# Optimization experiments

Hardware: AMD Instinct MI355X
Metric: run time of the kernel (lower is better)

Reference implementation:

```python
import jax, jax.numpy as jnp
import numpy as np

B, N = 2, 2048
TOP_K = 48
NUM_RBF = 16
MAX_REL = 32            # max_relative_feature
NUM_POS = 16            # num_positional_embeddings
EDGE_FEATURES = 128
EDGE_IN = NUM_POS + NUM_RBF * 25  # 416
POS_IN = 2 * MAX_REL + 2          # 66 one-hot classes


def setup_inputs() -> dict:
    key = jax.random.key(0)
    k0, k1, k2, k3 = jax.random.split(key, 4)
    X = jax.random.normal(k0, (B, N, 4, 3), dtype=jnp.float32) * 3.0
    mask = jnp.ones((B, N), dtype=jnp.float32)
    R_idx = jnp.arange(B * N, dtype=jnp.int32).reshape(B, N)
    chain_labels = jax.random.randint(k1, (B, N), 0, 4).astype(jnp.int32)
    W_pos = 0.05 * jax.random.normal(k2, (POS_IN, NUM_POS), dtype=jnp.float32)
    b_pos = jnp.zeros((NUM_POS,), dtype=jnp.float32)
    W_edge = 0.05 * jax.random.normal(k3, (EDGE_IN, EDGE_FEATURES), dtype=jnp.float32)
    b_edge = jnp.zeros((EDGE_FEATURES,), dtype=jnp.float32)
    return {"X": X, "mask": mask, "R_idx": R_idx, "chain_labels": chain_labels,
            "W_pos": W_pos, "b_pos": b_pos, "W_edge": W_edge, "b_edge": b_edge}


def _rbf(D):
    # D: [..., K] -> [..., K, NUM_RBF]
    mu = jnp.linspace(2.0, 22.0, NUM_RBF)        # D_min=2, D_max=22
    sigma = (22.0 - 2.0) / NUM_RBF               # 1.25
    return jnp.exp(-(((D[..., None] - mu) / sigma) ** 2))


def _pair_dist(A, Bc):
    # A, Bc: [B, N, 3] -> [B, N, N]
    return jnp.sqrt(jnp.sum((A[:, :, None, :] - Bc[:, None, :, :]) ** 2, axis=-1) + 1e-6)


def reference(X, mask, R_idx, chain_labels, W_pos, b_pos, W_edge, b_edge):
    # virtual Cbeta from backbone geometry
    b = X[:, :, 1, :] - X[:, :, 0, :]
    c = X[:, :, 2, :] - X[:, :, 1, :]
    a = jnp.cross(b, c, axis=-1)
    Cb = -0.58273431 * a + 0.56802827 * b - 0.54067466 * c + X[:, :, 1, :]
    Ca, Nat, Cat, Oat = X[:, :, 1, :], X[:, :, 0, :], X[:, :, 2, :], X[:, :, 3, :]

    # masked Ca-Ca distances + k nearest neighbors
    mask2 = mask[:, None, :] * mask[:, :, None]
    D = mask2 * _pair_dist(Ca, Ca)
    D_adjust = D + (1.0 - mask2) * jnp.max(D, axis=-1, keepdims=True)
    neg_D, E_idx = jax.lax.top_k(-D_adjust, min(TOP_K, N))  # smallest distances
    D_neighbors = -neg_D                                     # [B, N, K]

    rbfs = [_rbf(D_neighbors)]
    pairs = [(Nat, Nat), (Cat, Cat), (Oat, Oat), (Cb, Cb),
             (Ca, Nat), (Ca, Cat), (Ca, Oat), (Ca, Cb),
             (Nat, Cat), (Nat, Oat), (Nat, Cb), (Cb, Cat), (Cb, Oat), (Oat, Cat),
             (Nat, Ca), (Cat, Ca), (Oat, Ca), (Cb, Ca),
             (Cat, Nat), (Oat, Nat), (Cb, Nat), (Cat, Cb), (Oat, Cb), (Cat, Oat)]
    for A_, B_ in pairs:  # fixed structural set of 24 atom-pair types
        Dab = _pair_dist(A_, B_)                          # [B, N, N]
        Dn = jnp.take_along_axis(Dab, E_idx, axis=2)      # [B, N, K]
        rbfs.append(_rbf(Dn))
    RBF_all = jnp.concatenate(rbfs, axis=-1)              # [B, N, K, 25*NUM_RBF]

    # relative positional / chain features at the gathered neighbors
    offset = R_idx[:, :, None] - R_idx[:, None, :]
    offset = jnp.take_along_axis(offset, E_idx, axis=2)   # [B, N, K]
    d_chains = (chain_labels[:, :, None] == chain_labels[:, None, :]).astype(jnp.int32)
    E_chains = jnp.take_along_axis(d_chains, E_idx, axis=2)

    d = jnp.clip(offset + MAX_REL, 0, 2 * MAX_REL)
    d = d * E_chains + (1 - E_chains) * (2 * MAX_REL + 1)
    d_onehot = jax.nn.one_hot(d, POS_IN, dtype=jnp.float32)  # [B, N, K, 66]
    E_positional = d_onehot @ W_pos + b_pos                  # [B, N, K, 16]

    E = jnp.concatenate((E_positional, RBF_all), axis=-1)    # [B, N, K, 416]
    E = E @ W_edge + b_edge                                  # [B, N, K, 128]
    return E, E_idx
```

## Files before the change

### kernel.cpp

```cpp
#include <hip/hip_runtime.h>
#include <hip/hip_bf16.h>
#include <stdint.h>

#define BB   2
#define NN   2048
#define BN   (BB*NN)
#define KTOP 48
#define EIN  416
#define EF   128

typedef __attribute__((ext_vector_type(8))) short s8v;
typedef __attribute__((ext_vector_type(4))) float f32x4;
typedef __attribute__((ext_vector_type(4))) unsigned int u32x4;
typedef unsigned short u16;
typedef unsigned int u32;
typedef unsigned long long u64;

__device__ __constant__ int cPA[25] = {1,0,2,3,4,1,1,1,1,0,0,0,4,4,3,0,2,3,4,2,3,4,2,3,2};
__device__ __constant__ int cPB[25] = {1,0,2,3,4,0,2,3,4,2,3,4,2,3,2,1,1,1,1,0,0,0,4,4,3};

__device__ __forceinline__ u16 bf16u(float x) {
  __hip_bfloat16 h = __float2bfloat16(x);
  return *reinterpret_cast<u16*>(&h);
}
__device__ __forceinline__ u32 cvtpk(float lo, float hi) {
  u32 r;
  asm("v_cvt_pk_bf16_f32 %0, %1, %2" : "=v"(r) : "v"(lo), "v"(hi));
  return r;
}

__global__ __launch_bounds__(256) void prep_kernel(const float* __restrict__ X,
                                                   const float* __restrict__ W_edge,
                                                   float* __restrict__ atoms5p,
                                                   float* __restrict__ capack4,
                                                   u16* __restrict__ wtf) {
  int tid = blockIdx.x * 256 + threadIdx.x;
  if (tid < EIN * EF) {
    int k = tid >> 7, n = tid & 127;
    wtf[((size_t)(k >> 3)) * 1024 + n * 8 + (k & 7)] = bf16u(W_edge[tid]);
  } else if (tid < EIN * EF + BN) {
    int idx = tid - EIN * EF;
    const float* x = X + (size_t)idx * 12;
    float Nx = x[0], Ny = x[1], Nz = x[2];
    float Cax = x[3], Cay = x[4], Caz = x[5];
    float Cx = x[6], Cy = x[7], Cz = x[8];
    float Ox = x[9], Oy = x[10], Oz = x[11];
    float bx = Cax - Nx, by = Cay - Ny, bz = Caz - Nz;
    float cx = Cx - Cax, cy = Cy - Cay, cz = Cz - Caz;
    float ax = by * cz - bz * cy;
    float ay = bz * cx - bx * cz;
    float az = bx * cy - by * cx;
    float Cbx = -0.58273431f * ax + 0.56802827f * bx - 0.54067466f * cx + Cax;
    float Cby = -0.58273431f * ay + 0.56802827f * by - 0.54067466f * cy + Cay;
    float Cbz = -0.58273431f * az + 0.56802827f * bz - 0.54067466f * cz + Caz;
    f32x4* o = (f32x4*)(atoms5p + (size_t)idx * 20);
    o[0] = (f32x4){Nx, Ny, Nz, 0.f};
    o[1] = (f32x4){Cax, Cay, Caz, 0.f};
    o[2] = (f32x4){Cx, Cy, Cz, 0.f};
    o[3] = (f32x4){Ox, Oy, Oz, 0.f};
    o[4] = (f32x4){Cbx, Cby, Cbz, 0.f};
    *(f32x4*)(capack4 + (size_t)idx * 4) = (f32x4){Cax, Cay, Caz, 0.f};
  }
}

__device__ __forceinline__ u32 blockExclScan(u32 v, u32* scanw, int t) {
  int lane = t & 63, w = t >> 6;
  u32 inc = v;
#pragma unroll
  for (int off = 1; off < 64; off <<= 1) {
    u32 o = __shfl_up(inc, off);
    if (lane >= off) inc += o;
  }
  if (lane == 63) scanw[w] = inc;
  __syncthreads();
  u32 base = 0;
  for (int ww = 0; ww < w; ++ww) base += scanw[ww];
  __syncthreads();
  return base + inc - v;
}

template<int NB, bool CHKPREF>
__device__ __forceinline__ void radix_round(u32* hist, u32* scanw, u32* selinfo, int t,
                                            const u32* kv, u32 pref, int prefShift,
                                            int binShift, u32 binMask, u32 r) {
  const int PB = NB / 256;
#pragma unroll
  for (int q = 0; q < PB / 4; ++q)
    *(u32x4*)&hist[t * PB + q * 4] = (u32x4){0, 0, 0, 0};
  __syncthreads();
#pragma unroll
  for (int s = 0; s < 8; ++s) {
    bool ok = (!CHKPREF) || ((kv[s] >> prefShift) == pref);
    if (ok) atomicAdd(&hist[(kv[s] >> binShift) & binMask], 1u);
  }
  __syncthreads();
  u32 loc[PB];
  u32 sum = 0;
#pragma unroll
  for (int q = 0; q < PB / 4; ++q) {
    u32x4 lv = *(u32x4*)&hist[t * PB + q * 4];
    loc[q * 4 + 0] = lv.x; loc[q * 4 + 1] = lv.y;
    loc[q * 4 + 2] = lv.z; loc[q * 4 + 3] = lv.w;
    sum += lv.x + lv.y + lv.z + lv.w;
  }
  int lane = t & 63, w = t >> 6;
  u32 inc = sum;
#pragma unroll
  for (int off = 1; off < 64; off <<= 1) {
    u32 o = __shfl_up(inc, off);
    if (lane >= off) inc += o;
  }
  if (lane == 63) scanw[w] = inc;
  __syncthreads();
  u32 base = 0;
  for (int ww = 0; ww < w; ++ww) base += scanw[ww];
  u32 c = base + inc - sum;
#pragma unroll
  for (int q = 0; q < PB; ++q) {
    u32 nc = c + loc[q];
    if (c < r && r <= nc) { selinfo[0] = (u32)(t * PB + q); selinfo[1] = r - c; }
    c = nc;
  }
  __syncthreads();
}

__global__ __launch_bounds__(256) void topk_kernel(const float* __restrict__ capack4,
                                                   const float* __restrict__ mask,
                                                   float* __restrict__ dtop,
                                                   float* __restrict__ eidx_f) {
  __shared__ u32 hist[4096];
  __shared__ u32 scanw[4];
  __shared__ u32 selinfo[2];
  __shared__ float redf[4];
  __shared__ u64 win[64];

  int row = blockIdx.x;
  int b = row >> 11, i = row & (NN - 1);
  int t = threadIdx.x, lane = t & 63, w = t >> 6;
  const float* cab4 = capack4 + (size_t)b * NN * 4;
  const float* mrow = mask + (size_t)b * NN;
  f32x4 ci = *(const f32x4*)&cab4[(size_t)i * 4];
  float mi = mrow[i];
  f32x4 mk0 = *(const f32x4*)&mrow[t * 8];
  f32x4 mk1 = *(const f32x4*)&mrow[t * 8 + 4];

  float dvv[8], m2v[8];
  float lmax = 0.f;
#pragma unroll
  for (int s = 0; s < 8; ++s) {
    f32x4 cj = *(const f32x4*)&cab4[(size_t)(t * 8 + s) * 4];
    float dx = ci.x - cj.x, dy = ci.y - cj.y, dz = ci.z - cj.z;
    float d = sqrtf(dx * dx + dy * dy + dz * dz + 1e-6f);
    float mj = (s < 4) ? mk0[s] : mk1[s - 4];
    float m2 = mi * mj;
    float D = m2 * d;
    dvv[s] = D; m2v[s] = m2;
    lmax = fmaxf(lmax, D);
  }
#pragma unroll
  for (int off = 32; off >= 1; off >>= 1) lmax = fmaxf(lmax, __shfl_xor(lmax, off));
  if (lane == 0) redf[w] = lmax;
  __syncthreads();
  float rmax = fmaxf(fmaxf(redf[0], redf[1]), fmaxf(redf[2], redf[3]));

  u32 kv[8];
#pragma unroll
  for (int s = 0; s < 8; ++s)
    kv[s] = __float_as_uint(dvv[s] + (1.0f - m2v[s]) * rmax);

  u32 r = KTOP;
  radix_round<4096, false>(hist, scanw, selinfo, t, kv, 0, 0, 20, 0xFFFu, r);
  u32 sel1 = selinfo[0]; r = selinfo[1];
  radix_round<1024, true>(hist, scanw, selinfo, t, kv, sel1, 20, 10, 0x3FFu, r);
  u32 sel2 = selinfo[0]; r = selinfo[1];
  u32 pref12 = (sel1 << 10) | sel2;
  radix_round<1024, true>(hist, scanw, selinfo, t, kv, pref12, 10, 0, 0x3FFu, r);
  u32 sel3 = selinfo[0];
  u32 takeEq = selinfo[1];
  u32 T = (sel1 << 20) | (sel2 << 10) | sel3;

  u32 lcnt = 0, ecnt = 0;
#pragma unroll
  for (int s = 0; s < 8; ++s) { lcnt += (kv[s] < T); ecnt += (kv[s] == T); }
  u32 ebase = blockExclScan(ecnt, scanw, t);
  u32 taken = 0;
  if (ebase < takeEq) { u32 room = takeEq - ebase; taken = room < ecnt ? room : ecnt; }
  u32 wbase = blockExclScan(lcnt + taken, scanw, t);
  u32 slot = wbase, tleft = taken;
#pragma unroll
  for (int s = 0; s < 8; ++s) {
    u32 j = (u32)(t * 8 + s);
    if (kv[s] < T) {
      win[slot++] = ((u64)kv[s] << 32) | j;
    } else if (kv[s] == T && tleft) {
      win[slot++] = ((u64)kv[s] << 32) | j;
      tleft--;
    }
  }
  __syncthreads();

  if (w == 0) {
    u64 key = (lane < KTOP) ? win[lane] : ~0ull;
#pragma unroll
    for (int k = 2; k <= 64; k <<= 1) {
#pragma unroll
      for (int jj = k >> 1; jj >= 1; jj >>= 1) {
        u64 p = __shfl_xor(key, jj);
        bool lowerl = (lane & jj) == 0;
        bool asc = (lane & k) == 0;
        u64 mn = p < key ? p : key;
        u64 mx = p < key ? key : p;
        key = (lowerl == asc) ? mn : mx;
      }
    }
    if (lane < KTOP) {
      u32 j = (u32)(key & 0xffffffffu);
      eidx_f[row * KTOP + lane] = (float)j;
      dtop[row * KTOP + lane] = __uint_as_float((u32)(key >> 32));
    }
  }
}

__device__ __forceinline__ s8v rbf8(float D, float mu0) {
  float Dc = fminf(D, 40.0f);
  float t0 = (Dc - mu0) * 0.8f;
  float v0 = __expf(-t0 * t0);
  float g = __expf(fmaf(2.13333333f, t0, -1.13777778f));
  const float C = 0.10273985f;
  float v1 = v0 * g; g *= C;
  float v2 = v1 * g; g *= C;
  float v3 = v2 * g; g *= C;
  float v4 = v3 * g; g *= C;
  float v5 = v4 * g; g *= C;
  float v6 = v5 * g; g *= C;
  float v7 = v6 * g;
  union { u32x4 u; s8v s; } cv;
  cv.u = (u32x4){cvtpk(v0, v1), cvtpk(v2, v3), cvtpk(v4, v5), cvtpk(v6, v7)};
  return cv.s;
}

__global__ __launch_bounds__(64, 5) void edge_kernel(const float* __restrict__ atoms5p,
                                                     const u16* __restrict__ wtf,
                                                     const float* __restrict__ eidx_f,
                                                     const float* __restrict__ dtop,
                                                     const int* __restrict__ Ridx,
                                                     const int* __restrict__ chains,
                                                     const float* __restrict__ Wpos,
                                                     const float* __restrict__ bpos,
                                                     const float* __restrict__ bedge,
                                                     float* __restrict__ Eout) {
  __shared__ float D_lds[16][26];
  __shared__ u32 pos_lds[16][8];
  __shared__ int jbuf[16];
  __shared__ f32x4 aI_lds[5];

  int lane = threadIdx.x;
  int bid = blockIdx.x;
  int row = bid / 3, mt = bid - row * 3;
  int b = row >> 11, i = row & (NN - 1);
  int kbase = mt * 16;
  const float* atomsB = atoms5p + (size_t)b * NN * 20;

  if (lane < 5) aI_lds[lane] = *(const f32x4*)&atomsB[(size_t)i * 20 + lane * 4];
  if (lane < 16) {
    int k = kbase + lane;
    int j = (int)eidx_f[(size_t)row * KTOP + k];
    jbuf[lane] = j;
    D_lds[lane][0] = dtop[(size_t)row * KTOP + k];
    int Ri = Ridx[b * NN + i], Rj = Ridx[b * NN + j];
    int same = (chains[b * NN + i] == chains[b * NN + j]);
    int off = Ri - Rj + 32;
    off = off < 0 ? 0 : (off > 64 ? 64 : off);
    int drow = same ? off : 65;
    const float* wr = Wpos + drow * 16;
    u32 pk[8];
#pragma unroll
    for (int h = 0; h < 4; ++h) {
      f32x4 wv = *(const f32x4*)&wr[h * 4];
      f32x4 bv = *(const f32x4*)&bpos[h * 4];
      pk[h * 2 + 0] = cvtpk(wv.x + bv.x, wv.y + bv.y);
      pk[h * 2 + 1] = cvtpk(wv.z + bv.z, wv.w + bv.w);
    }
    *(u32x4*)&pos_lds[lane][0] = (u32x4){pk[0], pk[1], pk[2], pk[3]};
    *(u32x4*)&pos_lds[lane][4] = (u32x4){pk[4], pk[5], pk[6], pk[7]};
  }

#pragma unroll
  for (int q = 0; q < 6; ++q) {
    int e = q * 64 + lane;
    int kl = e / 24;
    int p = e - kl * 24 + 1;
    int j = jbuf[kl];
    f32x4 I = aI_lds[cPA[p]];
    f32x4 J = *(const f32x4*)&atomsB[(size_t)j * 20 + cPB[p] * 4];
    float dx = I.x - J.x, dy = I.y - J.y, dz = I.z - J.z;
    D_lds[kl][p] = __builtin_amdgcn_sqrtf(dx * dx + dy * dy + dz * dz + 1e-6f);
  }

  int lr = lane & 15, lg = lane >> 4;
  const u16* wk = wtf + (size_t)lg * 1024 + lr * 8;
  const float MU8 = 12.6666667f;
  f32x4 acc[8] = {};

  {
    s8v af;
    if (lg < 2) {
      af = *reinterpret_cast<const s8v*>(&pos_lds[lr][lg * 4]);
    } else {
      af = rbf8(D_lds[lr][0], (lg == 2) ? 2.0f : MU8);
    }
#pragma unroll
    for (int nt = 0; nt < 8; ++nt) {
      s8v bv = *reinterpret_cast<const s8v*>(wk + nt * 128);
      acc[nt] = __builtin_amdgcn_mfma_f32_16x16x32_bf16(af, bv, acc[nt], 0, 0, 0);
    }
  }
#pragma unroll
  for (int kc = 1; kc < 13; ++kc) {
    int p = 2 * kc - 1 + (lg >> 1);
    float mu0 = (lg & 1) ? MU8 : 2.0f;
    s8v af = rbf8(D_lds[lr][p], mu0);
    const u16* wkc = wk + (size_t)kc * 4096;
#pragma unroll
    for (int nt = 0; nt < 8; ++nt) {
      s8v bv = *reinterpret_cast<const s8v*>(wkc + nt * 128);
      acc[nt] = __builtin_amdgcn_mfma_f32_16x16x32_bf16(af, bv, acc[nt], 0, 0, 0);
    }
  }

  float bias[8];
#pragma unroll
  for (int nt = 0; nt < 8; ++nt) bias[nt] = bedge[nt * 16 + lr];
  float* orow = Eout + ((size_t)row * KTOP + kbase) * EF;
#pragma unroll
  for (int qq = 0; qq < 4; ++qq) {
    float* pr = orow + (size_t)(lg * 4 + qq) * EF + lr;
#pragma unroll
    for (int nt = 0; nt < 8; ++nt)
      pr[nt * 16] = acc[nt][qq] + bias[nt];
  }
}

extern "C" void kernel_launch(void* const* d_in, const int* in_sizes, int n_in,
                              void* d_out, int out_size, void* d_ws, size_t ws_size,
                              hipStream_t stream) {
  const float* X = (const float*)d_in[0];
  const float* mask = (const float*)d_in[1];
  const int* Ridx = (const int*)d_in[2];
  const int* chains = (const int*)d_in[3];
  const float* Wpos = (const float*)d_in[4];
  const float* bpos = (const float*)d_in[5];
  const float* Wedge = (const float*)d_in[6];
  const float* bedge = (const float*)d_in[7];

  float* Eout = (float*)d_out;
  float* EidxF = Eout + (size_t)BN * KTOP * EF;

  u16* wtf = (u16*)d_ws;
  float* atoms5p = (float*)((char*)d_ws + 53248 * 2);
  float* capack4 = atoms5p + (size_t)BN * 20;
  float* dtop = capack4 + (size_t)BN * 4;

  prep_kernel<<<(EIN * EF + BN + 255) / 256, 256, 0, stream>>>(X, Wedge, atoms5p, capack4, wtf);
  topk_kernel<<<BN, 256, 0, stream>>>(capack4, mask, dtop, EidxF);
  edge_kernel<<<BN * 3, 64, 0, stream>>>(atoms5p, wtf, EidxF, dtop, Ridx, chains, Wpos, bpos, bedge, Eout);
}
```

Before: 95.65 us.

## Share LDS-staged weight tiles across four waves with double-buffered async loads

The edge kernel now runs four independent 16-neighbor tasks per 256-thread block. The bf16 weight chunks are staged into a double-buffered LDS tile with global_load_lds, so the four waves share them instead of each reading them from global/L2. Per-lane distance and positional-feature computation moves into registers, removing the earlier LDS staging and its associated work. The cost is a __syncthreads per K-chunk and more register pressure from holding 12 distances and the atom coordinates per lane.

```diff
diff --git a/kernel.cpp b/kernel.cpp
--- a/kernel.cpp
+++ b/kernel.cpp
@@ -239,93 +239,98 @@
   return cv.s;
 }
 
-__global__ __launch_bounds__(64, 5) void edge_kernel(const float* __restrict__ atoms5p,
-                                                     const u16* __restrict__ wtf,
-                                                     const float* __restrict__ eidx_f,
-                                                     const float* __restrict__ dtop,
-                                                     const int* __restrict__ Ridx,
-                                                     const int* __restrict__ chains,
-                                                     const float* __restrict__ Wpos,
-                                                     const float* __restrict__ bpos,
-                                                     const float* __restrict__ bedge,
-                                                     float* __restrict__ Eout) {
-  __shared__ float D_lds[16][26];
-  __shared__ u32 pos_lds[16][8];
-  __shared__ int jbuf[16];
-  __shared__ f32x4 aI_lds[5];
-
-  int lane = threadIdx.x;
-  int bid = blockIdx.x;
-  int row = bid / 3, mt = bid - row * 3;
+#define STAGE(bufi, kcs) do {                                                        \
+  const u16* _s = wtf + (kcs) * 4096 + t * 8;                                        \
+  __builtin_amdgcn_global_load_lds(                                                  \
+      (const __attribute__((address_space(1))) u32*)_s,                              \
+      (__attribute__((address_space(3))) u32*)&bbuf[bufi][t * 8], 16, 0, 0);         \
+  __builtin_amdgcn_global_load_lds(                                                  \
+      (const __attribute__((address_space(1))) u32*)(_s + 2048),                     \
+      (__attribute__((address_space(3))) u32*)&bbuf[bufi][t * 8 + 2048], 16, 0, 0);  \
+} while (0)
+
+__global__ __launch_bounds__(256, 4) void edge_kernel(const float* __restrict__ atoms5p,
+                                                      const u16* __restrict__ wtf,
+                                                      const float* __restrict__ eidx_f,
+                                                      const float* __restrict__ dtop,
+                                                      const int* __restrict__ Ridx,
+                                                      const int* __restrict__ chains,
+                                                      const float* __restrict__ Wpos,
+                                                      const float* __restrict__ bpos,
+                                                      const float* __restrict__ bedge,
+                                                      float* __restrict__ Eout) {
+  __shared__ __align__(16) u16 bbuf[2][4096];
+
+  static constexpr int kPA[25] = {1,0,2,3,4,1,1,1,1,0,0,0,4,4,3,0,2,3,4,2,3,4,2,3,2};
+  static constexpr int kPB[25] = {1,0,2,3,4,0,2,3,4,2,3,4,2,3,2,1,1,1,1,0,0,0,4,4,3};
+
+  int t = threadIdx.x;
+  int lane = t & 63, w = t >> 6;
+  int lr = lane & 15, lg = lane >> 4;
+
+  int task = blockIdx.x * 4 + w;
+  int row = task / 3, mt = task - row * 3;
   int b = row >> 11, i = row & (NN - 1);
   int kbase = mt * 16;
   const float* atomsB = atoms5p + (size_t)b * NN * 20;
 
-  if (lane < 5) aI_lds[lane] = *(const f32x4*)&atomsB[(size_t)i * 20 + lane * 4];
-  if (lane < 16) {
-    int k = kbase + lane;
-    int j = (int)eidx_f[(size_t)row * KTOP + k];
-    jbuf[lane] = j;
-    D_lds[lane][0] = dtop[(size_t)row * KTOP + k];
+  int kk = kbase + lr;
+  int j = (int)eidx_f[(size_t)row * KTOP + kk];
+  float dtv = dtop[(size_t)row * KTOP + kk];
+
+  f32x4 I[5], J[5];
+#pragma unroll
+  for (int a = 0; a < 5; ++a) {
+    I[a] = *(const f32x4*)&atomsB[(size_t)i * 20 + a * 4];
+    J[a] = *(const f32x4*)&atomsB[(size_t)j * 20 + a * 4];
+  }
+
+  bool hi = (lg >= 2);
+  float D[12];
+#pragma unroll
+  for (int q = 0; q < 12; ++q) {
+    int pO = 2 * q + 1, pE = 2 * q + 2;
+    f32x4 Iv = hi ? I[kPA[pE]] : I[kPA[pO]];
+    f32x4 Jv = hi ? J[kPB[pE]] : J[kPB[pO]];
+    float dx = Iv.x - Jv.x, dy = Iv.y - Jv.y, dz = Iv.z - Jv.z;
+    D[q] = __builtin_amdgcn_sqrtf(dx * dx + dy * dy + dz * dz + 1e-6f);
+  }
+
+  const float MU8 = 12.6666667f;
+  s8v af0;
+  if (lg < 2) {
     int Ri = Ridx[b * NN + i], Rj = Ridx[b * NN + j];
     int same = (chains[b * NN + i] == chains[b * NN + j]);
     int off = Ri - Rj + 32;
     off = off < 0 ? 0 : (off > 64 ? 64 : off);
     int drow = same ? off : 65;
-    const float* wr = Wpos + drow * 16;
-    u32 pk[8];
-#pragma unroll
-    for (int h = 0; h < 4; ++h) {
-      f32x4 wv = *(const f32x4*)&wr[h * 4];
-      f32x4 bv = *(const f32x4*)&bpos[h * 4];
-      pk[h * 2 + 0] = cvtpk(wv.x + bv.x, wv.y + bv.y);
-      pk[h * 2 + 1] = cvtpk(wv.z + bv.z, wv.w + bv.w);
-    }
-    *(u32x4*)&pos_lds[lane][0] = (u32x4){pk[0], pk[1], pk[2], pk[3]};
-    *(u32x4*)&pos_lds[lane][4] = (u32x4){pk[4], pk[5], pk[6], pk[7]};
-  }
-
-#pragma unroll
-  for (int q = 0; q < 6; ++q) {
-    int e = q * 64 + lane;
-    int kl = e / 24;
-    int p = e - kl * 24 + 1;
-    int j = jbuf[kl];
-    f32x4 I = aI_lds[cPA[p]];
-    f32x4 J = *(const f32x4*)&atomsB[(size_t)j * 20 + cPB[p] * 4];
-    float dx = I.x - J.x, dy = I.y - J.y, dz = I.z - J.z;
-    D_lds[kl][p] = __builtin_amdgcn_sqrtf(dx * dx + dy * dy + dz * dz + 1e-6f);
-  }
-
-  int lr = lane & 15, lg = lane >> 4;
-  const u16* wk = wtf + (size_t)lg * 1024 + lr * 8;
-  const float MU8 = 12.6666667f;
+    const float* wr = Wpos + drow * 16 + lg * 8;
+    f32x4 w0 = *(const f32x4*)wr;
+    f32x4 w1 = *(const f32x4*)(wr + 4);
+    f32x4 b0 = *(const f32x4*)(bpos + lg * 8);
+    f32x4 b1 = *(const f32x4*)(bpos + lg * 8 + 4);
+    union { u32x4 u; s8v s; } cv;
+    cv.u = (u32x4){cvtpk(w0.x + b0.x, w0.y + b0.y), cvtpk(w0.z + b0.z, w0.w + b0.w),
+                   cvtpk(w1.x + b1.x, w1.y + b1.y), cvtpk(w1.z + b1.z, w1.w + b1.w)};
+    af0 = cv.s;
+  } else {
+    af0 = rbf8(dtv, (lg == 2) ? 2.0f : MU8);
+  }
+
   f32x4 acc[8] = {};
-
-  {
-    s8v af;
-    if (lg < 2) {
-      af = *reinterpret_cast<const s8v*>(&pos_lds[lr][lg * 4]);
-    } else {
-      af = rbf8(D_lds[lr][0], (lg == 2) ? 2.0f : MU8);
-    }
+  STAGE(0, 0);
+  __syncthreads();
+#pragma unroll
+  for (int kc = 0; kc < 13; ++kc) {
+    if (kc < 12) STAGE((kc + 1) & 1, kc + 1);
+    s8v af = (kc == 0) ? af0 : rbf8(D[kc - 1], (lg & 1) ? MU8 : 2.0f);
+    const u16* bb = &bbuf[kc & 1][lg * 1024 + lr * 8];
 #pragma unroll
     for (int nt = 0; nt < 8; ++nt) {
-      s8v bv = *reinterpret_cast<const s8v*>(wk + nt * 128);
+      s8v bv = *(const s8v*)(bb + nt * 128);
       acc[nt] = __builtin_amdgcn_mfma_f32_16x16x32_bf16(af, bv, acc[nt], 0, 0, 0);
     }
-  }
-#pragma unroll
-  for (int kc = 1; kc < 13; ++kc) {
-    int p = 2 * kc - 1 + (lg >> 1);
-    float mu0 = (lg & 1) ? MU8 : 2.0f;
-    s8v af = rbf8(D_lds[lr][p], mu0);
-    const u16* wkc = wk + (size_t)kc * 4096;
-#pragma unroll
-    for (int nt = 0; nt < 8; ++nt) {
-      s8v bv = *reinterpret_cast<const s8v*>(wkc + nt * 128);
-      acc[nt] = __builtin_amdgcn_mfma_f32_16x16x32_bf16(af, bv, acc[nt], 0, 0, 0);
-    }
+    __syncthreads();
   }
 
   float bias[8];
@@ -363,5 +368,5 @@
 
   prep_kernel<<<(EIN * EF + BN + 255) / 256, 256, 0, stream>>>(X, Wedge, atoms5p, capack4, wtf);
   topk_kernel<<<BN, 256, 0, stream>>>(capack4, mask, dtop, EidxF);
-  edge_kernel<<<BN * 3, 64, 0, stream>>>(atoms5p, wtf, EidxF, dtop, Ridx, chains, Wpos, bpos, bedge, Eout);
-}
+  edge_kernel<<<BN * 3 / 4, 256, 0, stream>>>(atoms5p, wtf, EidxF, dtop, Ridx, chains, Wpos, bpos, bedge, Eout);
+}
```

Measured after the change: 115.4 us. 1.21x slower.
